# Kernel optimization log

Hardware: AMD Instinct MI355X
Metric: run time of the kernel (lower is better)

## Reference

```python
import jax, jax.numpy as jnp
import numpy as np

B, C = 2_000_000, 16


def setup_inputs() -> dict:
    key = jax.random.key(0)
    k1, k2 = jax.random.split(key)
    output = jax.random.normal(k1, (B, C), dtype=jnp.float32)
    score = jax.random.uniform(k2, (B,), dtype=jnp.float32)
    return {"output": output, "score": score}


def reference(output, score):
    # softmax over classes; top-1 value and index per row
    probs = jax.nn.softmax(output, axis=1)          # [B, C]
    prob_val = jnp.max(probs, axis=1)               # [B]
    prob_idx = jnp.argmax(probs, axis=1)            # [B]

    # select rows whose predicted top class is 0, preserving batch order.
    # jit-friendly: stable-sort selected rows to the front instead of boolean indexing.
    mask = prob_idx == 0                            # [B] bool
    order = jnp.argsort(jnp.logical_not(mask), stable=True)  # selected first, original order kept
    p = prob_val[order]                             # [B]
    s = score[order]                                # [B]
    n = jnp.sum(mask)                               # number of selected rows

    # adjacent-pair ranking loss over the first n entries:
    # sum_i log(1 + exp(-(p_i - p_{i+1}) * sign(s_i - s_{i+1})))
    tmp = (p[:-1] - p[1:]) * jnp.sign(s[:-1] - s[1:])        # [B-1]
    valid = jnp.arange(p.shape[0] - 1) < (n - 1)             # pairs fully inside selected prefix
    reg_term = jnp.sum(jnp.where(valid, jnp.log1p(jnp.exp(-tmp)), jnp.zeros_like(tmp)))
    return reg_term
```

## Files before the change

### kernel.cpp

```cpp
#include <hip/hip_runtime.h>

#define TPB 256
#define NW  (TPB / 64)

__device__ __forceinline__ float pair_loss(float p0, float s0, float p1, float s1) {
    float dp = p0 - p1;
    float ds = s0 - s1;
    float sg = (ds > 0.0f) ? 1.0f : ((ds < 0.0f) ? -1.0f : 0.0f);
    float t  = dp * sg;
    return fmaxf(-t, 0.0f) + log1pf(__expf(-fabsf(t)));
}

__device__ __forceinline__ void row_stats(const float* __restrict__ outp, int row,
                                          float& p, bool& mask) {
    const float4* o4 = (const float4*)outp + (size_t)row * 4;
    float4 a = o4[0];
    float4 b = o4[1];
    float4 c = o4[2];
    float4 d = o4[3];
    float m01 = fmaxf(fmaxf(a.x, a.y), fmaxf(a.z, a.w));
    float m23 = fmaxf(fmaxf(b.x, b.y), fmaxf(b.z, b.w));
    float m45 = fmaxf(fmaxf(c.x, c.y), fmaxf(c.z, c.w));
    float m67 = fmaxf(fmaxf(d.x, d.y), fmaxf(d.z, d.w));
    float m = fmaxf(fmaxf(m01, m23), fmaxf(m45, m67));
    float sum = __expf(a.x - m) + __expf(a.y - m) + __expf(a.z - m) + __expf(a.w - m)
              + __expf(b.x - m) + __expf(b.y - m) + __expf(b.z - m) + __expf(b.w - m)
              + __expf(c.x - m) + __expf(c.y - m) + __expf(c.z - m) + __expf(c.w - m)
              + __expf(d.x - m) + __expf(d.y - m) + __expf(d.z - m) + __expf(d.w - m);
    p = 1.0f / sum;
    mask = (a.x == m);
}

__global__ void k_fused(const float* __restrict__ outp,
                        const float* __restrict__ score,
                        float* __restrict__ bpart, int B) {
    __shared__ float sp[TPB];
    __shared__ float ss[TPB];
    __shared__ unsigned long long wmask[NW];
    __shared__ float wsum[NW];

    int row  = blockIdx.x * TPB + threadIdx.x;
    int lane = threadIdx.x & 63;
    int wid  = threadIdx.x >> 6;

    bool mask = false;
    float p = 0.0f, s = 0.0f;
    if (row < B) {
        row_stats(outp, row, p, mask);
        s = score[row];
    }
    sp[threadIdx.x] = p;
    ss[threadIdx.x] = s;

    unsigned long long bal = __ballot(mask);
    if (lane == 0) wmask[wid] = bal;
    __syncthreads();

    float acc = 0.0f;
    if (mask) {
        unsigned long long above = bal & ~((2ull << lane) - 1ull);
        int nxt = -1;
        if (above) {
            nxt = (wid << 6) + __ffsll(above) - 1;
        } else {
            for (int w = wid + 1; w < NW; ++w) {
                if (wmask[w]) { nxt = (w << 6) + __ffsll(wmask[w]) - 1; break; }
            }
        }
        if (nxt >= 0) acc = pair_loss(p, s, sp[nxt], ss[nxt]);
    }

    if (wid == 0) {
        int last = -1;
        for (int w = NW - 1; w >= 0; --w) {
            if (wmask[w]) { last = (w << 6) + 63 - __clzll(wmask[w]); break; }
        }
        if (last >= 0) {
            float pl = sp[last];
            float sl = ss[last];
            int base = (blockIdx.x + 1) * TPB;
            while (base < B) {
                int r = base + lane;
                bool sel = false;
                float pf = 0.0f, sf = 0.0f;
                if (r < B) {
                    row_stats(outp, r, pf, sel);
                    sf = score[r];
                }
                unsigned long long b2 = __ballot(sel);
                if (b2) {
                    int fl = __ffsll(b2) - 1;
                    float pfirst = __shfl(pf, fl);
                    float sfirst = __shfl(sf, fl);
                    if (lane == 0) acc += pair_loss(pl, sl, pfirst, sfirst);
                    break;
                }
                base += 64;
            }
        }
    }

    for (int off = 32; off > 0; off >>= 1) acc += __shfl_down(acc, off);
    if (lane == 0) wsum[wid] = acc;
    __syncthreads();
    if (threadIdx.x == 0) {
        bpart[blockIdx.x] = wsum[0] + wsum[1] + wsum[2] + wsum[3];
    }
}

__global__ void k2_sum(const float* __restrict__ bpart, int nb,
                       float* __restrict__ out) {
    __shared__ float wsum[16];
    float acc = 0.0f;
    for (int b = threadIdx.x; b < nb; b += 1024) acc += bpart[b];
    int lane = threadIdx.x & 63;
    int wid  = threadIdx.x >> 6;
    for (int off = 32; off > 0; off >>= 1) acc += __shfl_down(acc, off);
    if (lane == 0) wsum[wid] = acc;
    __syncthreads();
    if (threadIdx.x == 0) {
        float t = 0.0f;
        for (int w = 0; w < 16; ++w) t += wsum[w];
        out[0] = t;
    }
}

extern "C" void kernel_launch(void* const* d_in, const int* in_sizes, int n_in,
                              void* d_out, int out_size, void* d_ws, size_t ws_size,
                              hipStream_t stream) {
    const float* outp  = (const float*)d_in[0];
    const float* score = (const float*)d_in[1];
    float* out = (float*)d_out;

    int B  = in_sizes[1];
    int nb = (B + TPB - 1) / TPB;

    float* bpart = (float*)d_ws;

    k_fused<<<nb, TPB, 0, stream>>>(outp, score, bpart, B);
    k2_sum<<<1, 1024, 0, stream>>>(bpart, nb, out);
}
```

Before: 36.07 us.

## Process four rows per thread with packed nibble masks and fewer blocks

Each thread now handles four consecutive rows, loads their scores as one float4, and builds the block's selection bitmask by packing per-thread nibbles through shared memory instead of using wave ballots. The grid shrinks fourfold, which cuts the per-block overhead, the cross-block lookahead scans, and the partial sums the second kernel must reduce. The reciprocal is switched to the hardware rcp intrinsic. In exchange, each thread's loads are strided (64 contiguous bytes per row across four rows) and there is an extra barrier plus a serial nibble-packing step.

```diff
diff --git a/kernel.cpp b/kernel.cpp
--- a/kernel.cpp
+++ b/kernel.cpp
@@ -1,7 +1,9 @@
 #include <hip/hip_runtime.h>
 
-#define TPB 256
-#define NW  (TPB / 64)
+#define TPB   256
+#define ROWS  4
+#define RPB   (TPB * ROWS)
+#define NWORD (RPB / 64)
 
 __device__ __forceinline__ float pair_loss(float p0, float s0, float p1, float s1) {
     float dp = p0 - p1;
@@ -27,58 +29,77 @@
               + __expf(b.x - m) + __expf(b.y - m) + __expf(b.z - m) + __expf(b.w - m)
               + __expf(c.x - m) + __expf(c.y - m) + __expf(c.z - m) + __expf(c.w - m)
               + __expf(d.x - m) + __expf(d.y - m) + __expf(d.z - m) + __expf(d.w - m);
-    p = 1.0f / sum;
+    p = __builtin_amdgcn_rcpf(sum);
     mask = (a.x == m);
 }
 
-__global__ void k_fused(const float* __restrict__ outp,
-                        const float* __restrict__ score,
-                        float* __restrict__ bpart, int B) {
-    __shared__ float sp[TPB];
-    __shared__ float ss[TPB];
-    __shared__ unsigned long long wmask[NW];
-    __shared__ float wsum[NW];
+__global__ void __launch_bounds__(TPB) k_fused(const float* __restrict__ outp,
+                                               const float* __restrict__ score,
+                                               float* __restrict__ bpart, int B) {
+    __shared__ float sp[RPB];
+    __shared__ float ss[RPB];
+    __shared__ unsigned char nib[TPB];
+    __shared__ unsigned long long wmask[NWORD];
+    __shared__ float wsum[TPB / 64];
 
-    int row  = blockIdx.x * TPB + threadIdx.x;
-    int lane = threadIdx.x & 63;
-    int wid  = threadIdx.x >> 6;
+    int tid  = threadIdx.x;
+    int lane = tid & 63;
+    int wid  = tid >> 6;
+    int blk0 = blockIdx.x * RPB;
+    int r0   = blk0 + tid * ROWS;
 
-    bool mask = false;
-    float p = 0.0f, s = 0.0f;
-    if (row < B) {
-        row_stats(outp, row, p, mask);
-        s = score[row];
+    float p[ROWS], sc[ROWS];
+    bool  mk[ROWS];
+    unsigned int mynib = 0;
+
+    if (r0 + ROWS <= B) {
+        float4 s4 = ((const float4*)score)[blk0 / 4 + tid];
+        sc[0] = s4.x; sc[1] = s4.y; sc[2] = s4.z; sc[3] = s4.w;
+    } else {
+        for (int j = 0; j < ROWS; ++j) sc[j] = (r0 + j < B) ? score[r0 + j] : 0.0f;
     }
-    sp[threadIdx.x] = p;
-    ss[threadIdx.x] = s;
+    for (int j = 0; j < ROWS; ++j) {
+        p[j] = 0.0f; mk[j] = false;
+        if (r0 + j < B) row_stats(outp, r0 + j, p[j], mk[j]);
+        sp[tid * ROWS + j] = p[j];
+        ss[tid * ROWS + j] = sc[j];
+        if (mk[j]) mynib |= 1u << j;
+    }
+    nib[tid] = (unsigned char)mynib;
+    __syncthreads();
 
-    unsigned long long bal = __ballot(mask);
-    if (lane == 0) wmask[wid] = bal;
+    if (tid < NWORD) {
+        unsigned long long w = 0;
+        for (int k = 0; k < 16; ++k)
+            w |= (unsigned long long)(nib[tid * 16 + k] & 0xF) << (4 * k);
+        wmask[tid] = w;
+    }
     __syncthreads();
 
     float acc = 0.0f;
-    if (mask) {
-        unsigned long long above = bal & ~((2ull << lane) - 1ull);
+    for (int j = 0; j < ROWS; ++j) {
+        if (!mk[j]) continue;
+        int i  = tid * ROWS + j;
+        int w0 = i >> 6, b0 = i & 63;
+        unsigned long long above = wmask[w0] & ~((2ull << b0) - 1ull);
         int nxt = -1;
         if (above) {
-            nxt = (wid << 6) + __ffsll(above) - 1;
+            nxt = (w0 << 6) + __ffsll(above) - 1;
         } else {
-            for (int w = wid + 1; w < NW; ++w) {
+            for (int w = w0 + 1; w < NWORD; ++w)
                 if (wmask[w]) { nxt = (w << 6) + __ffsll(wmask[w]) - 1; break; }
-            }
         }
-        if (nxt >= 0) acc = pair_loss(p, s, sp[nxt], ss[nxt]);
+        if (nxt >= 0) acc += pair_loss(p[j], sc[j], sp[nxt], ss[nxt]);
     }
 
     if (wid == 0) {
         int last = -1;
-        for (int w = NW - 1; w >= 0; --w) {
+        for (int w = NWORD - 1; w >= 0; --w)
             if (wmask[w]) { last = (w << 6) + 63 - __clzll(wmask[w]); break; }
-        }
         if (last >= 0) {
             float pl = sp[last];
             float sl = ss[last];
-            int base = (blockIdx.x + 1) * TPB;
+            int base = blk0 + RPB;
             while (base < B) {
                 int r = base + lane;
                 bool sel = false;
@@ -103,9 +124,8 @@
     for (int off = 32; off > 0; off >>= 1) acc += __shfl_down(acc, off);
     if (lane == 0) wsum[wid] = acc;
     __syncthreads();
-    if (threadIdx.x == 0) {
+    if (tid == 0)
         bpart[blockIdx.x] = wsum[0] + wsum[1] + wsum[2] + wsum[3];
-    }
 }
 
 __global__ void k2_sum(const float* __restrict__ bpart, int nb,
@@ -133,7 +153,7 @@
     float* out = (float*)d_out;
 
     int B  = in_sizes[1];
-    int nb = (B + TPB - 1) / TPB;
+    int nb = (B + RPB - 1) / RPB;
 
     float* bpart = (float*)d_ws;
 
```

After: 38.04 us. 5.4% more time.
